# Kernel optimization log

Hardware: AMD Instinct MI355X
Metric: run time of the kernel (lower is better)

## Reference

```python
import jax, jax.numpy as jnp
import numpy as np

EPS = 1e-5  # torch LayerNorm default


def setup_inputs() -> dict:
    key = jax.random.key(0)
    ks = jax.random.split(key, 6)
    B, C, H, W, D = 8, 128, 64, 64, 32
    x = jax.random.normal(ks[0], (B, C, H, W), dtype=jnp.float32)
    gamma = jnp.ones((C,), dtype=jnp.float32)
    beta = jnp.zeros((C,), dtype=jnp.float32)
    Wq = jax.random.normal(ks[1], (D, C), dtype=jnp.float32) * 0.02
    Wk = jax.random.normal(ks[2], (D, C), dtype=jnp.float32) * 0.02
    Wv = jax.random.normal(ks[3], (C, C), dtype=jnp.float32) * 0.02
    Wo = jax.random.normal(ks[4], (C, C), dtype=jnp.float32) * (1.0 / np.sqrt(C))
    bo = jnp.zeros((C,), dtype=jnp.float32)
    return {"x": x, "gamma": gamma, "beta": beta, "Wq": Wq, "Wk": Wk,
            "Wv": Wv, "Wo": Wo, "bo": bo}


def reference(x, gamma, beta, Wq, Wk, Wv, Wo, bo):
    B, C, H, W = x.shape
    # LayerNorm over channel dim (applied in NHWC in the original)
    xn = x.transpose(0, 2, 3, 1)                       # [B,H,W,C]
    mu = xn.mean(-1, keepdims=True)
    var = ((xn - mu) ** 2).mean(-1, keepdims=True)
    xn = (xn - mu) * jax.lax.rsqrt(var + EPS) * gamma + beta
    xn = xn.transpose(0, 3, 1, 2)                      # [B,C,H,W]
    # 1x1-conv projections == channel matmuls
    q = jnp.einsum('dc,bchw->bdhw', Wq, xn)
    k = jnp.einsum('dc,bchw->bdhw', Wk, xn)
    v = jnp.einsum('oc,bchw->bohw', Wv, xn)
    # full spatial attention: scores [B,H,W,H,W], softmax over key positions
    scores = jnp.einsum('bchw,bcxy->bhwxy', q, k)
    scores = scores.reshape(B, H, W, H * W)
    attn = jax.nn.softmax(scores, axis=-1).reshape(B, H, W, H, W)
    out = jnp.einsum('bhwxy,bcxy->bchw', attn, v)
    out = jnp.einsum('oc,bchw->bohw', Wo, out) + bo[None, :, None, None]
    return out + x
```

## Files before the change

### kernel.cpp

```cpp
#include <hip/hip_runtime.h>


#define NB 8
#define CCH 128
#define NTOK 4096
#define DQK 32
#define KT 64

typedef __attribute__((ext_vector_type(8))) short bf16x8;
typedef __attribute__((ext_vector_type(4))) float f32x4;
typedef unsigned short u16;
typedef unsigned int u32;

static __device__ __forceinline__ f32x4 mfma16(bf16x8 a, bf16x8 b, f32x4 c) {
  return __builtin_amdgcn_mfma_f32_16x16x32_bf16(a, b, c, 0, 0, 0);
}
static __device__ __forceinline__ u16 f2bf(float f) {
  union { float f; u32 u; } cv; cv.f = f;
  u32 u = cv.u;
  u += 0x7fffu + ((u >> 16) & 1u);
  return (u16)(u >> 16);
}
static __device__ __forceinline__ float bf2f(u16 v) {
  union { u32 u; float f; } cv; cv.u = ((u32)v) << 16;
  return cv.f;
}
static __device__ __forceinline__ u32 cvtpk(float lo, float hi) {
  u32 d;
  asm("v_cvt_pk_bf16_f32 %0, %1, %2" : "=v"(d) : "v"(lo), "v"(hi));
  return d;
}
static __device__ __forceinline__ void gload16(const void* g, void* l) {
  __builtin_amdgcn_global_load_lds(
      (const __attribute__((address_space(1))) void*)g,
      (__attribute__((address_space(3))) void*)l, 16, 0, 0);
}

__global__ __launch_bounds__(256) void wconv_kernel(
    const float* __restrict__ Wq, const float* __restrict__ Wk,
    const float* __restrict__ Wv, const float* __restrict__ Wo,
    u16* __restrict__ wcomb) {
  int idx = blockIdx.x * 256 + threadIdx.x;
  int r = idx >> 7;
  float v;
  if (r < 32)        v = Wq[idx];
  else if (r < 64)   v = Wk[idx - 4096];
  else if (r < 192)  v = Wv[idx - 8192];
  else               v = Wo[idx - 24576];
  wcomb[idx] = f2bf(v);
}

__global__ __launch_bounds__(256) void lnqkv_kernel(
    const float* __restrict__ x, const float* __restrict__ gamma,
    const float* __restrict__ beta, const u16* __restrict__ wcomb,
    u16* __restrict__ Qg, u16* __restrict__ Kg, u16* __restrict__ Vt) {
  __shared__ float tile[128][64];
  __shared__ float red[2][4][64];
  __shared__ u16   xt[64][130];
  int t = threadIdx.x;
  int lane = t & 63, cq = t >> 6;
  int b = blockIdx.x >> 6;
  int posb = (blockIdx.x & 63) << 6;
  const float* xb = x + ((size_t)b * CCH) * NTOK + posb;
  for (int i = 0; i < 32; ++i) {
    int c = cq * 32 + i;
    tile[c][lane] = xb[(size_t)c * NTOK + lane];
  }
  __syncthreads();
  float s = 0.f, s2 = 0.f;
  for (int i = 0; i < 32; ++i) {
    float v = tile[cq * 32 + i][lane];
    s += v; s2 += v * v;
  }
  red[0][cq][lane] = s; red[1][cq][lane] = s2;
  __syncthreads();
  float mu  = (red[0][0][lane] + red[0][1][lane] + red[0][2][lane] + red[0][3][lane]) * (1.f / 128.f);
  float ex2 = (red[1][0][lane] + red[1][1][lane] + red[1][2][lane] + red[1][3][lane]) * (1.f / 128.f);
  float rstd = rsqrtf(ex2 - mu * mu + 1e-5f);
  for (int i = 0; i < 32; ++i) {
    int c = cq * 32 + i;
    float v = (tile[c][lane] - mu) * rstd * gamma[c] + beta[c];
    xt[lane][c] = f2bf(v);
  }
  __syncthreads();
  int w = t >> 6, row16 = lane & 15, kgrp = lane >> 4;
  bf16x8 af[4];
  for (int ks = 0; ks < 4; ++ks)
    af[ks] = *(const bf16x8*)&xt[w * 16 + row16][ks * 32 + kgrp * 8];
  f32x4 zero = {0.f, 0.f, 0.f, 0.f};
  f32x4 acc[12];
  for (int nt = 0; nt < 12; ++nt) {
    acc[nt] = zero;
    for (int ks = 0; ks < 4; ++ks) {
      bf16x8 bf = *(const bf16x8*)&wcomb[(size_t)(nt * 16 + row16) * CCH + ks * 32 + kgrp * 8];
      acc[nt] = mfma16(af[ks], bf, acc[nt]);
    }
  }
  int tok0 = b * NTOK + posb;
  for (int nt = 0; nt < 12; ++nt) {
    int col = nt * 16 + row16;
    for (int r = 0; r < 4; ++r) {
      int token = tok0 + w * 16 + kgrp * 4 + r;
      if (col < 32) {
        Qg[(size_t)token * DQK + col] = f2bf(acc[nt][r] * 1.44269504f);
      } else if (col < 64) {
        Kg[(size_t)token * DQK + (col - 32)] = f2bf(acc[nt][r]);
      } else {
        int tl = token & (NTOK - 1);
        int kp = (tl & ~31) | ((tl & 12) << 1) | ((tl & 16) >> 2) | (tl & 3);
        Vt[((size_t)b * CCH + (col - 64)) * NTOK + kp] = f2bf(acc[nt][r]);
      }
    }
  }
}

template <int NS>
__global__ __launch_bounds__(256, 4) void attn_kernel(
    const u16* __restrict__ Qg, const u16* __restrict__ Kg,
    const u16* __restrict__ Vt, u16* __restrict__ Op,
    float* __restrict__ lp) {
  __shared__ u16 lds[2][10240];
  constexpr int KSEG = NTOK / NS;
  constexpr int NTILE = KSEG / KT;
  constexpr int BSH = (NS == 4) ? 7 : 6;
  int t = threadIdx.x;
  int w = t >> 6, lane = t & 63;
  int row16 = lane & 15, kgrp = lane >> 4;

  int cpx = (256 * NS) >> 3;
  int logical = (blockIdx.x & 7) * cpx + (blockIdx.x >> 3);
  int qblk = logical & 31;
  int part = (logical >> 5) & (NS - 1);
  int b = logical >> BSH;
  int q0 = qblk * 128;
  int kt0 = part * KSEG;

  const u16* Qb = Qg + ((size_t)(b * NTOK + q0 + w * 32)) * DQK;
  bf16x8 qf0 = *(const bf16x8*)&Qb[(size_t)row16 * DQK + kgrp * 8];
  bf16x8 qf1 = *(const bf16x8*)&Qb[(size_t)(16 + row16) * DQK + kgrp * 8];

  bf16x8 ones_b;
  {
    short one = (short)0x3F80;
    short val = (row16 == 0) ? one : (short)0;
    for (int j = 0; j < 8; ++j) ones_b[j] = val;
  }

  int pr = t >> 3, e8 = t & 7;
  int korig = e8 ^ (pr & 7);
  int kkey = pr * 2 + (korig >> 2);
  int kfs = korig & 3;
  const u16* ksrc = Kg + (size_t)(b * NTOK + kt0 + kkey) * DQK + kfs * 8;
  int cV = t >> 3;
  int sV = e8 ^ (cV & 7);
  const u16* vsrc = Vt + ((size_t)b * CCH + cV) * NTOK + kt0 + sV * 8;

  int kdst = w * 512;
  int vdst = w * 512;

  f32x4 zero = {0.f, 0.f, 0.f, 0.f};
  f32x4 o0[8], o1[8], ol0, ol1;
#pragma unroll
  for (int i = 0; i < 8; ++i) { o0[i] = zero; o1[i] = zero; }
  ol0 = zero; ol1 = zero;

  auto stage = [&](int bi, int tile) {
    const u16* kp_ = ksrc + (size_t)tile * (KT * DQK);
    gload16(kp_, &lds[bi][kdst]);
    const u16* vp_ = vsrc + tile * KT;
    gload16(vp_,          &lds[bi][2048 + vdst]);
    gload16(vp_ + 131072, &lds[bi][2048 + 2048 + vdst]);
    gload16(vp_ + 262144, &lds[bi][2048 + 4096 + vdst]);
    gload16(vp_ + 393216, &lds[bi][2048 + 6144 + vdst]);
  };

  auto compute = [&](int bi) {
    const u16* kb = &lds[bi][0];
    const u16* vb = &lds[bi][2048];
    f32x4 sa0[4], sa1[4];
#pragma unroll
    for (int nt = 0; nt < 4; ++nt) {
      int slot = (nt * 8 + (row16 >> 1)) * 8 +
                 ((((row16 & 1) << 2) + kgrp) ^ (row16 >> 1));
      bf16x8 kf = *(const bf16x8*)&kb[slot * 8];
      sa0[nt] = mfma16(kf, qf0, zero);
      sa1[nt] = mfma16(kf, qf1, zero);
    }
#pragma unroll
    for (int nt = 0; nt < 4; ++nt)
      for (int r = 0; r < 4; ++r) {
        sa0[nt][r] = __builtin_amdgcn_exp2f(sa0[nt][r]);
        sa1[nt][r] = __builtin_amdgcn_exp2f(sa1[nt][r]);
      }
    union PU { u32 d[4]; bf16x8 v; };
    PU pf0[2], pf1[2];
#pragma unroll
    for (int ks = 0; ks < 2; ++ks) {
      pf0[ks].d[0] = cvtpk(sa0[2 * ks][0], sa0[2 * ks][1]);
      pf0[ks].d[1] = cvtpk(sa0[2 * ks][2], sa0[2 * ks][3]);
      pf0[ks].d[2] = cvtpk(sa0[2 * ks + 1][0], sa0[2 * ks + 1][1]);
      pf0[ks].d[3] = cvtpk(sa0[2 * ks + 1][2], sa0[2 * ks + 1][3]);
      pf1[ks].d[0] = cvtpk(sa1[2 * ks][0], sa1[2 * ks][1]);
      pf1[ks].d[1] = cvtpk(sa1[2 * ks][2], sa1[2 * ks][3]);
      pf1[ks].d[2] = cvtpk(sa1[2 * ks + 1][0], sa1[2 * ks + 1][1]);
      pf1[ks].d[3] = cvtpk(sa1[2 * ks + 1][2], sa1[2 * ks + 1][3]);
    }
    ol0 = mfma16(pf0[0].v, ones_b, ol0);
    ol0 = mfma16(pf0[1].v, ones_b, ol0);
    ol1 = mfma16(pf1[0].v, ones_b, ol1);
    ol1 = mfma16(pf1[1].v, ones_b, ol1);
#pragma unroll
    for (int ks = 0; ks < 2; ++ks)
#pragma unroll
      for (int ntc = 0; ntc < 8; ++ntc) {
        int vslot = (ntc * 16 + row16) * 8 + (((ks << 2) + kgrp) ^ (row16 & 7));
        bf16x8 vf = *(const bf16x8*)&vb[vslot * 8];
        o0[ntc] = mfma16(pf0[ks].v, vf, o0[ntc]);
        o1[ntc] = mfma16(pf1[ks].v, vf, o1[ntc]);
      }
  };

  stage(0, 0);
  asm volatile("s_waitcnt vmcnt(0)" ::: "memory");
  __builtin_amdgcn_s_barrier();
  int cur = 0;
  for (int tile = 0; tile < NTILE - 1; ++tile) {
    stage(cur ^ 1, tile + 1);
    compute(cur);
    asm volatile("s_waitcnt vmcnt(0)" ::: "memory");
    __builtin_amdgcn_s_barrier();
    cur ^= 1;
  }
  compute(cur);

  u16* Opw = Op + (size_t)part * (32768 * CCH);
  int tokb = b * NTOK + q0 + w * 32;
#pragma unroll
  for (int r = 0; r < 4; ++r) {
    int tk0 = tokb + kgrp * 4 + r;
    int tk1 = tokb + 16 + kgrp * 4 + r;
#pragma unroll
    for (int ntc = 0; ntc < 8; ++ntc) {
      Opw[(size_t)tk0 * CCH + ntc * 16 + row16] = f2bf(o0[ntc][r]);
      Opw[(size_t)tk1 * CCH + ntc * 16 + row16] = f2bf(o1[ntc][r]);
    }
  }
  if (row16 == 0) {
#pragma unroll
    for (int r = 0; r < 4; ++r) {
      lp[part * 32768 + tokb + kgrp * 4 + r] = ol0[r];
      lp[part * 32768 + tokb + 16 + kgrp * 4 + r] = ol1[r];
    }
  }
}

__global__ __launch_bounds__(256) void out_kernel(
    const u16* __restrict__ Op, const float* __restrict__ lp, int ns,
    const u16* __restrict__ wcomb, const float* __restrict__ bo,
    const float* __restrict__ x, float* __restrict__ out) {
  int t = threadIdx.x;
  int w = t >> 6, lane = t & 63;
  int row16 = lane & 15, kgrp = lane >> 4;
  int tok0 = blockIdx.x * 64;
  int b = tok0 >> 12, tloc = tok0 & (NTOK - 1);
  int tokA = tok0 + w * 16 + row16;
  float lsum = 0.f;
  for (int j = 0; j < ns; ++j) lsum += lp[j * 32768 + tokA];
  float inv = 1.f / lsum;
  bf16x8 af[4];
  for (int ks = 0; ks < 4; ++ks) {
    float sum[8] = {0.f, 0.f, 0.f, 0.f, 0.f, 0.f, 0.f, 0.f};
    for (int j = 0; j < ns; ++j) {
      bf16x8 a = *(const bf16x8*)&Op[(size_t)j * (32768 * CCH) +
                                     (size_t)tokA * CCH + ks * 32 + kgrp * 8];
      for (int e = 0; e < 8; ++e) sum[e] += bf2f((u16)a[e]);
    }
    bf16x8 av;
    for (int e = 0; e < 8; ++e) av[e] = (short)f2bf(sum[e] * inv);
    af[ks] = av;
  }
  f32x4 zero = {0.f, 0.f, 0.f, 0.f};
  f32x4 acc[8];
  for (int nt = 0; nt < 8; ++nt) {
    acc[nt] = zero;
    for (int ks = 0; ks < 4; ++ks) {
      bf16x8 bf = *(const bf16x8*)&wcomb[(size_t)(192 + nt * 16 + row16) * CCH + ks * 32 + kgrp * 8];
      acc[nt] = mfma16(af[ks], bf, acc[nt]);
    }
  }
  for (int nt = 0; nt < 8; ++nt) {
    int cout = nt * 16 + row16;
    float bias = bo[cout];
    size_t base = ((size_t)b * CCH + cout) * NTOK + tloc + w * 16 + kgrp * 4;
    float4 xr = *(const float4*)&x[base];
    float4 ov;
    ov.x = acc[nt][0] + bias + xr.x;
    ov.y = acc[nt][1] + bias + xr.y;
    ov.z = acc[nt][2] + bias + xr.z;
    ov.w = acc[nt][3] + bias + xr.w;
    *(float4*)&out[base] = ov;
  }
}

extern "C" void kernel_launch(void* const* d_in, const int* in_sizes, int n_in,
                              void* d_out, int out_size, void* d_ws, size_t ws_size,
                              hipStream_t stream) {
  const float* x     = (const float*)d_in[0];
  const float* gamma = (const float*)d_in[1];
  const float* beta  = (const float*)d_in[2];
  const float* Wq    = (const float*)d_in[3];
  const float* Wk    = (const float*)d_in[4];
  const float* Wv    = (const float*)d_in[5];
  const float* Wo    = (const float*)d_in[6];
  const float* bo    = (const float*)d_in[7];
  float* out = (float*)d_out;

  unsigned char* ws = (unsigned char*)d_ws;
  u16* Qg    = (u16*)(ws);
  u16* Kg    = (u16*)(ws + 2097152);
  u16* Vt    = (u16*)(ws + 4194304);
  u16* wcomb = (u16*)(ws + 12582912);
  float* lp  = (float*)(ws + 12664832);
  u16* Op    = (u16*)(ws + 13189120);

  int ns = (ws_size >= 46743552u) ? 4 : 2;

  wconv_kernel<<<160, 256, 0, stream>>>(Wq, Wk, Wv, Wo, wcomb);
  lnqkv_kernel<<<512, 256, 0, stream>>>(x, gamma, beta, wcomb, Qg, Kg, Vt);
  if (ns == 4)
    attn_kernel<4><<<1024, 256, 0, stream>>>(Qg, Kg, Vt, Op, lp);
  else
    attn_kernel<2><<<512, 256, 0, stream>>>(Qg, Kg, Vt, Op, lp);
  out_kernel<<<512, 256, 0, stream>>>(Op, lp, ns, wcomb, bo, x, out);
}
```

Baseline: 93.34 us.

## Shrink attention blocks to 2 waves and key tiles to 32 keys

The attention kernel now runs 128-thread blocks covering 64 queries, launching twice as many blocks. Each K/V tile holds 32 keys instead of 64, with reworked LDS swizzles and staging for the smaller V tile. The aim is finer-grained scheduling and more resident blocks through smaller LDS use. In exchange, each loaded K/V tile is reused by fewer query rows, so global traffic doubles and there are twice as many barriers per key segment.

New measurement: 96.36 us. 3.2% more time.

```diff
diff --git a/kernel.cpp b/kernel.cpp
--- a/kernel.cpp
+++ b/kernel.cpp
@@ -5,7 +5,7 @@
 #define CCH 128
 #define NTOK 4096
 #define DQK 32
-#define KT 64
+#define KT 32
 
 typedef __attribute__((ext_vector_type(8))) short bf16x8;
 typedef __attribute__((ext_vector_type(4))) float f32x4;
@@ -115,24 +115,23 @@
 }
 
 template <int NS>
-__global__ __launch_bounds__(256, 4) void attn_kernel(
+__global__ __launch_bounds__(128, 4) void attn_kernel(
     const u16* __restrict__ Qg, const u16* __restrict__ Kg,
     const u16* __restrict__ Vt, u16* __restrict__ Op,
     float* __restrict__ lp) {
-  __shared__ u16 lds[2][10240];
+  __shared__ u16 lds[2][5120];
   constexpr int KSEG = NTOK / NS;
   constexpr int NTILE = KSEG / KT;
-  constexpr int BSH = (NS == 4) ? 7 : 6;
   int t = threadIdx.x;
   int w = t >> 6, lane = t & 63;
   int row16 = lane & 15, kgrp = lane >> 4;
 
-  int cpx = (256 * NS) >> 3;
+  int cpx = (512 * NS) >> 3;
   int logical = (blockIdx.x & 7) * cpx + (blockIdx.x >> 3);
-  int qblk = logical & 31;
-  int part = (logical >> 5) & (NS - 1);
-  int b = logical >> BSH;
-  int q0 = qblk * 128;
+  int qblk = logical & 63;
+  int part = (logical >> 6) & (NS - 1);
+  int b = logical / (64 * NS);
+  int q0 = qblk * 64;
   int kt0 = part * KSEG;
 
   const u16* Qb = Qg + ((size_t)(b * NTOK + q0 + w * 32)) * DQK;
@@ -141,22 +140,18 @@
 
   bf16x8 ones_b;
   {
-    short one = (short)0x3F80;
-    short val = (row16 == 0) ? one : (short)0;
+    short val = (row16 == 0) ? (short)0x3F80 : (short)0;
     for (int j = 0; j < 8; ++j) ones_b[j] = val;
   }
 
-  int pr = t >> 3, e8 = t & 7;
-  int korig = e8 ^ (pr & 7);
+  int pr = t >> 3, d8 = t & 7;
+  int korig = d8 ^ (pr & 7);
   int kkey = pr * 2 + (korig >> 2);
   int kfs = korig & 3;
   const u16* ksrc = Kg + (size_t)(b * NTOK + kt0 + kkey) * DQK + kfs * 8;
-  int cV = t >> 3;
-  int sV = e8 ^ (cV & 7);
+  int cV = t >> 2;
+  int sV = (t & 3) ^ ((t >> 3) & 3);
   const u16* vsrc = Vt + ((size_t)b * CCH + cV) * NTOK + kt0 + sV * 8;
-
-  int kdst = w * 512;
-  int vdst = w * 512;
 
   f32x4 zero = {0.f, 0.f, 0.f, 0.f};
   f32x4 o0[8], o1[8], ol0, ol1;
@@ -166,20 +161,20 @@
 
   auto stage = [&](int bi, int tile) {
     const u16* kp_ = ksrc + (size_t)tile * (KT * DQK);
-    gload16(kp_, &lds[bi][kdst]);
+    gload16(kp_, &lds[bi][w * 512]);
     const u16* vp_ = vsrc + tile * KT;
-    gload16(vp_,          &lds[bi][2048 + vdst]);
-    gload16(vp_ + 131072, &lds[bi][2048 + 2048 + vdst]);
-    gload16(vp_ + 262144, &lds[bi][2048 + 4096 + vdst]);
-    gload16(vp_ + 393216, &lds[bi][2048 + 6144 + vdst]);
+#pragma unroll
+    for (int j = 0; j < 4; ++j)
+      gload16(vp_ + (size_t)j * (32 * NTOK),
+              &lds[bi][1024 + j * 1024 + w * 512]);
   };
 
   auto compute = [&](int bi) {
     const u16* kb = &lds[bi][0];
-    const u16* vb = &lds[bi][2048];
-    f32x4 sa0[4], sa1[4];
-#pragma unroll
-    for (int nt = 0; nt < 4; ++nt) {
+    const u16* vb = &lds[bi][1024];
+    f32x4 sa0[2], sa1[2];
+#pragma unroll
+    for (int nt = 0; nt < 2; ++nt) {
       int slot = (nt * 8 + (row16 >> 1)) * 8 +
                  ((((row16 & 1) << 2) + kgrp) ^ (row16 >> 1));
       bf16x8 kf = *(const bf16x8*)&kb[slot * 8];
@@ -187,37 +182,31 @@
       sa1[nt] = mfma16(kf, qf1, zero);
     }
 #pragma unroll
-    for (int nt = 0; nt < 4; ++nt)
+    for (int nt = 0; nt < 2; ++nt)
       for (int r = 0; r < 4; ++r) {
         sa0[nt][r] = __builtin_amdgcn_exp2f(sa0[nt][r]);
         sa1[nt][r] = __builtin_amdgcn_exp2f(sa1[nt][r]);
       }
     union PU { u32 d[4]; bf16x8 v; };
-    PU pf0[2], pf1[2];
-#pragma unroll
-    for (int ks = 0; ks < 2; ++ks) {
-      pf0[ks].d[0] = cvtpk(sa0[2 * ks][0], sa0[2 * ks][1]);
-      pf0[ks].d[1] = cvtpk(sa0[2 * ks][2], sa0[2 * ks][3]);
-      pf0[ks].d[2] = cvtpk(sa0[2 * ks + 1][0], sa0[2 * ks + 1][1]);
-      pf0[ks].d[3] = cvtpk(sa0[2 * ks + 1][2], sa0[2 * ks + 1][3]);
-      pf1[ks].d[0] = cvtpk(sa1[2 * ks][0], sa1[2 * ks][1]);
-      pf1[ks].d[1] = cvtpk(sa1[2 * ks][2], sa1[2 * ks][3]);
-      pf1[ks].d[2] = cvtpk(sa1[2 * ks + 1][0], sa1[2 * ks + 1][1]);
-      pf1[ks].d[3] = cvtpk(sa1[2 * ks + 1][2], sa1[2 * ks + 1][3]);
-    }
-    ol0 = mfma16(pf0[0].v, ones_b, ol0);
-    ol0 = mfma16(pf0[1].v, ones_b, ol0);
-    ol1 = mfma16(pf1[0].v, ones_b, ol1);
-    ol1 = mfma16(pf1[1].v, ones_b, ol1);
-#pragma unroll
-    for (int ks = 0; ks < 2; ++ks)
-#pragma unroll
-      for (int ntc = 0; ntc < 8; ++ntc) {
-        int vslot = (ntc * 16 + row16) * 8 + (((ks << 2) + kgrp) ^ (row16 & 7));
-        bf16x8 vf = *(const bf16x8*)&vb[vslot * 8];
-        o0[ntc] = mfma16(pf0[ks].v, vf, o0[ntc]);
-        o1[ntc] = mfma16(pf1[ks].v, vf, o1[ntc]);
-      }
+    PU pf0, pf1;
+    pf0.d[0] = cvtpk(sa0[0][0], sa0[0][1]);
+    pf0.d[1] = cvtpk(sa0[0][2], sa0[0][3]);
+    pf0.d[2] = cvtpk(sa0[1][0], sa0[1][1]);
+    pf0.d[3] = cvtpk(sa0[1][2], sa0[1][3]);
+    pf1.d[0] = cvtpk(sa1[0][0], sa1[0][1]);
+    pf1.d[1] = cvtpk(sa1[0][2], sa1[0][3]);
+    pf1.d[2] = cvtpk(sa1[1][0], sa1[1][1]);
+    pf1.d[3] = cvtpk(sa1[1][2], sa1[1][3]);
+    ol0 = mfma16(pf0.v, ones_b, ol0);
+    ol1 = mfma16(pf1.v, ones_b, ol1);
+#pragma unroll
+    for (int ntc = 0; ntc < 8; ++ntc) {
+      int c = ntc * 16 + row16;
+      int vslot = c * 4 + (kgrp ^ ((c >> 1) & 3));
+      bf16x8 vf = *(const bf16x8*)&vb[vslot * 8];
+      o0[ntc] = mfma16(pf0.v, vf, o0[ntc]);
+      o1[ntc] = mfma16(pf1.v, vf, o1[ntc]);
+    }
   };
 
   stage(0, 0);
@@ -328,8 +317,8 @@
   wconv_kernel<<<160, 256, 0, stream>>>(Wq, Wk, Wv, Wo, wcomb);
   lnqkv_kernel<<<512, 256, 0, stream>>>(x, gamma, beta, wcomb, Qg, Kg, Vt);
   if (ns == 4)
-    attn_kernel<4><<<1024, 256, 0, stream>>>(Qg, Kg, Vt, Op, lp);
+    attn_kernel<4><<<2048, 128, 0, stream>>>(Qg, Kg, Vt, Op, lp);
   else
-    attn_kernel<2><<<512, 256, 0, stream>>>(Qg, Kg, Vt, Op, lp);
+    attn_kernel<2><<<1024, 128, 0, stream>>>(Qg, Kg, Vt, Op, lp);
   out_kernel<<<512, 256, 0, stream>>>(Op, lp, ns, wcomb, bo, x, out);
 }
```
